# Kernel optimization log

Hardware: AMD Instinct MI355X
Metric: run time of the kernel (lower is better)

Reference implementation:

```python
import jax, jax.numpy as jnp
import numpy as np

GROUP = 128  # quantization group size along the input dimension


def dequant(q, scales, zeros):
    # q: [out, in] int4 codes stored as int32 in [0,16)
    # scales, zeros: [out, in//GROUP] per-group affine params
    out_dim, in_dim = q.shape
    g = in_dim // GROUP
    w = (q.astype(jnp.float32).reshape(out_dim, g, GROUP) - zeros[:, :, None]) * scales[:, :, None]
    return w.reshape(out_dim, in_dim)


def setup_inputs() -> dict:
    key = jax.random.key(0)
    ks = jax.random.split(key, 10)
    H, I = 4096, 11008
    B, S = 64, 1
    inp = {
        "x": jax.random.normal(ks[0], (B, S, H), dtype=jnp.float32),
        "gate_qweight": jax.random.randint(ks[1], (I, H), 0, 16, dtype=jnp.int32),
        "gate_scales": jax.random.uniform(ks[2], (I, H // GROUP), dtype=jnp.float32) * 0.02,
        "gate_zeros": jax.random.uniform(ks[3], (I, H // GROUP), dtype=jnp.float32) * 16.0,
        "up_qweight": jax.random.randint(ks[4], (I, H), 0, 16, dtype=jnp.int32),
        "up_scales": jax.random.uniform(ks[5], (I, H // GROUP), dtype=jnp.float32) * 0.02,
        "up_zeros": jax.random.uniform(ks[6], (I, H // GROUP), dtype=jnp.float32) * 16.0,
        "down_qweight": jax.random.randint(ks[7], (H, I), 0, 16, dtype=jnp.int32),
        "down_scales": jax.random.uniform(ks[8], (H, I // GROUP), dtype=jnp.float32) * 0.02,
        "down_zeros": jax.random.uniform(ks[9], (H, I // GROUP), dtype=jnp.float32) * 16.0,
    }
    return inp


def reference(x, gate_qweight, gate_scales, gate_zeros,
              up_qweight, up_scales, up_zeros,
              down_qweight, down_scales, down_zeros):
    Wg = dequant(gate_qweight, gate_scales, gate_zeros)   # [I, H]
    Wu = dequant(up_qweight, up_scales, up_zeros)         # [I, H]
    Wd = dequant(down_qweight, down_scales, down_zeros)   # [H, I]
    gate = jnp.einsum('bsh,ih->bsi', x, Wg)
    up = jnp.einsum('bsh,ih->bsi', x, Wu)
    h = jax.nn.silu(gate) * up                             # SwiGLU
    return jnp.einsum('bsi,hi->bsh', h, Wd)
```

## Files before the change

kernel.cpp:

```cpp
#include <hip/hip_runtime.h>
#include <hip/hip_bf16.h>
#include <stdint.h>

#define H_DIM 4096
#define I_DIM 11008
#define NGH   (H_DIM/128)
#define NGI   (I_DIM/128)

typedef __attribute__((ext_vector_type(8))) short short8;
typedef __attribute__((ext_vector_type(4))) short s16x4;
typedef __attribute__((ext_vector_type(4))) float f32x4;
typedef __attribute__((ext_vector_type(4))) int   i32x4;

static __device__ __forceinline__ short f2bf(float f) {
  union { __hip_bfloat16 b; short s; } u;
  u.b = __float2bfloat16(f);
  return u.s;
}

__global__ void xcvt_kernel(const float* __restrict__ x, short* __restrict__ xb) {
  int i = (blockIdx.x * 256 + threadIdx.x) * 4;
  f32x4 v = *(const f32x4*)(x + i);
  s16x4 o;
  o[0] = f2bf(v[0]); o[1] = f2bf(v[1]); o[2] = f2bf(v[2]); o[3] = f2bf(v[3]);
  *(s16x4*)(xb + i) = o;
}

__global__ __launch_bounds__(512, 4) void phase1_kernel(
    const short* __restrict__ xb,
    const int* __restrict__ gq, const float* __restrict__ gsc, const float* __restrict__ gze,
    const int* __restrict__ uq, const float* __restrict__ usc, const float* __restrict__ uze,
    short* __restrict__ hb)
{
  __shared__ float red[8][4][4][64];
  const int n0   = blockIdx.x * 16;
  const int w    = threadIdx.x >> 6;
  const int l    = threadIdx.x & 63;
  const int col  = l & 15;
  const int krow = l >> 4;
  const int i    = n0 + col;

  const int*   gqr = gq + (size_t)i * H_DIM;
  const int*   uqr = uq + (size_t)i * H_DIM;
  const float* gsr = gsc + (size_t)i * NGH;
  const float* gzr = gze + (size_t)i * NGH;
  const float* usr = usc + (size_t)i * NGH;
  const float* uzr = uze + (size_t)i * NGH;

  f32x4 accG[4], accU[4];
#pragma unroll
  for (int c = 0; c < 4; ++c)
#pragma unroll
    for (int r = 0; r < 4; ++r) { accG[c][r] = 0.f; accU[c][r] = 0.f; }

  const int kw = w * 512;

  int pk = kw + krow * 8;
  i32x4 nq0 = *(const i32x4*)(gqr + pk);
  i32x4 nq1 = *(const i32x4*)(gqr + pk + 4);
  i32x4 np0 = *(const i32x4*)(uqr + pk);
  i32x4 np1 = *(const i32x4*)(uqr + pk + 4);

#pragma unroll 1
  for (int g = 0; g < 4; ++g) {
    const int gg = w * 4 + g;
    const float sg = gsr[gg], zg = gzr[gg] * sg;
    const float su = usr[gg], zu = uzr[gg] * su;
#pragma unroll
    for (int ks = 0; ks < 4; ++ks) {
      i32x4 q0 = nq0, q1 = nq1, p0 = np0, p1 = np1;
      const int klocal = g * 128 + ks * 32;
      {
        const int nk = kw + ((klocal + 32) & 511) + krow * 8;
        nq0 = *(const i32x4*)(gqr + nk);
        nq1 = *(const i32x4*)(gqr + nk + 4);
        np0 = *(const i32x4*)(uqr + nk);
        np1 = *(const i32x4*)(uqr + nk + 4);
      }
      const int koff = kw + klocal + krow * 8;
      short8 a[4];
#pragma unroll
      for (int c = 0; c < 4; ++c)
        a[c] = *(const short8*)(xb + (size_t)(c * 16 + col) * H_DIM + koff);
      short8 bg, bu;
#pragma unroll
      for (int j = 0; j < 4; ++j) {
        bg[j]     = f2bf((float)q0[j] * sg - zg);
        bg[j + 4] = f2bf((float)q1[j] * sg - zg);
        bu[j]     = f2bf((float)p0[j] * su - zu);
        bu[j + 4] = f2bf((float)p1[j] * su - zu);
      }
#pragma unroll
      for (int c = 0; c < 4; ++c) {
        accG[c] = __builtin_amdgcn_mfma_f32_16x16x32_bf16(a[c], bg, accG[c], 0, 0, 0);
        accU[c] = __builtin_amdgcn_mfma_f32_16x16x32_bf16(a[c], bu, accU[c], 0, 0, 0);
      }
    }
  }

  const int c2 = threadIdx.x >> 7;
  const int rh = (threadIdx.x >> 6) & 1;
  const int ll = threadIdx.x & 63;

#pragma unroll
  for (int c = 0; c < 4; ++c)
#pragma unroll
    for (int r = 0; r < 4; ++r)
      red[w][c][r][l] = accG[c][r];
  __syncthreads();
  float gsum[2];
#pragma unroll
  for (int rr = 0; rr < 2; ++rr) {
    const int r = rh * 2 + rr;
    float s = 0.f;
#pragma unroll
    for (int ww = 0; ww < 8; ++ww) s += red[ww][c2][r][ll];
    gsum[rr] = s;
  }
  __syncthreads();

#pragma unroll
  for (int c = 0; c < 4; ++c)
#pragma unroll
    for (int r = 0; r < 4; ++r)
      red[w][c][r][l] = accU[c][r];
  __syncthreads();
#pragma unroll
  for (int rr = 0; rr < 2; ++rr) {
    const int r = rh * 2 + rr;
    float us = 0.f;
#pragma unroll
    for (int ww = 0; ww < 8; ++ww) us += red[ww][c2][r][ll];
    const float gv = gsum[rr];
    const float hv = gv / (1.f + __expf(-gv)) * us;
    const int m  = c2 * 16 + (ll >> 4) * 4 + r;
    const int ii = n0 + (ll & 15);
    hb[(size_t)m * I_DIM + ii] = f2bf(hv);
  }
}

__global__ __launch_bounds__(512, 4) void phase2_kernel(
    const short* __restrict__ hb,
    const int* __restrict__ dq, const float* __restrict__ dsc, const float* __restrict__ dze,
    float* __restrict__ part)
{
  __shared__ float red[8][4][4][64];
  const int tile  = blockIdx.x & 255;
  const int split = blockIdx.x >> 8;
  const int n0   = tile * 16;
  const int w    = threadIdx.x >> 6;
  const int l    = threadIdx.x & 63;
  const int col  = l & 15;
  const int krow = l >> 4;
  const int n    = n0 + col;

  const int*   dqr = dq + (size_t)n * I_DIM;
  const float* dsr = dsc + (size_t)n * NGI;
  const float* dzr = dze + (size_t)n * NGI;

  f32x4 acc[4];
#pragma unroll
  for (int c = 0; c < 4; ++c)
#pragma unroll
    for (int r = 0; r < 4; ++r) acc[c][r] = 0.f;

  const int cnt    = (w < 6) ? 11 : 10;
  const int sstart = (w < 6) ? w * 11 : 66 + (w - 6) * 10;
  const int kbase  = split * 2752 + sstart * 32;

  int gprev = -1;
  float sv = 0.f, zv = 0.f;

  int pk = kbase + krow * 8;
  i32x4 nq0 = *(const i32x4*)(dqr + pk);
  i32x4 nq1 = *(const i32x4*)(dqr + pk + 4);

#pragma unroll 1
  for (int s = 0; s < cnt; ++s) {
    i32x4 q0 = nq0, q1 = nq1;
    {
      const int ns = (s + 1 < cnt) ? (s + 1) : 0;
      const int nk = kbase + ns * 32 + krow * 8;
      nq0 = *(const i32x4*)(dqr + nk);
      nq1 = *(const i32x4*)(dqr + nk + 4);
    }
    const int k0 = kbase + s * 32;
    const int g  = k0 >> 7;
    if (g != gprev) { sv = dsr[g]; zv = dzr[g] * sv; gprev = g; }
    short8 a[4];
#pragma unroll
    for (int c = 0; c < 4; ++c)
      a[c] = *(const short8*)(hb + (size_t)(c * 16 + col) * I_DIM + k0 + krow * 8);
    short8 b;
#pragma unroll
    for (int j = 0; j < 4; ++j) {
      b[j]     = f2bf((float)q0[j] * sv - zv);
      b[j + 4] = f2bf((float)q1[j] * sv - zv);
    }
#pragma unroll
    for (int c = 0; c < 4; ++c)
      acc[c] = __builtin_amdgcn_mfma_f32_16x16x32_bf16(a[c], b, acc[c], 0, 0, 0);
  }

#pragma unroll
  for (int c = 0; c < 4; ++c)
#pragma unroll
    for (int r = 0; r < 4; ++r)
      red[w][c][r][l] = acc[c][r];
  __syncthreads();

  {
    const int c2 = threadIdx.x >> 7;
    const int rh = (threadIdx.x >> 6) & 1;
    const int ll = threadIdx.x & 63;
    float* po = part + (size_t)split * (64 * H_DIM);
#pragma unroll
    for (int rr = 0; rr < 2; ++rr) {
      const int r = rh * 2 + rr;
      float s = 0.f;
#pragma unroll
      for (int ww = 0; ww < 8; ++ww) s += red[ww][c2][r][ll];
      const int m  = c2 * 16 + (ll >> 4) * 4 + r;
      const int nn = n0 + (ll & 15);
      po[(size_t)m * H_DIM + nn] = s;
    }
  }
}

__global__ void reduce4_kernel(const float* __restrict__ part, float* __restrict__ out) {
  const int idx = (blockIdx.x * 256 + threadIdx.x) * 4;
  const int S = 64 * H_DIM;
  f32x4 s0 = *(const f32x4*)(part + idx);
  f32x4 s1 = *(const f32x4*)(part + S + idx);
  f32x4 s2 = *(const f32x4*)(part + 2 * S + idx);
  f32x4 s3 = *(const f32x4*)(part + 3 * S + idx);
  f32x4 r = (s0 + s1) + (s2 + s3);
  *(f32x4*)(out + idx) = r;
}

extern "C" void kernel_launch(void* const* d_in, const int* in_sizes, int n_in,
                              void* d_out, int out_size, void* d_ws, size_t ws_size,
                              hipStream_t stream) {
  const float* x  = (const float*)d_in[0];
  const int*   gq = (const int*)d_in[1];
  const float* gs = (const float*)d_in[2];
  const float* gz = (const float*)d_in[3];
  const int*   uq = (const int*)d_in[4];
  const float* us = (const float*)d_in[5];
  const float* uz = (const float*)d_in[6];
  const int*   dq = (const int*)d_in[7];
  const float* ds = (const float*)d_in[8];
  const float* dz = (const float*)d_in[9];
  float* out = (float*)d_out;

  short* xb = (short*)d_ws;
  short* hb = (short*)((char*)d_ws + (size_t)64 * H_DIM * 2);
  float* part = (float*)((char*)d_ws + (size_t)64 * H_DIM * 2 + (size_t)64 * I_DIM * 2);

  xcvt_kernel<<<(64 * H_DIM) / 1024, 256, 0, stream>>>(x, xb);
  phase1_kernel<<<I_DIM / 16, 512, 0, stream>>>(xb, gq, gs, gz, uq, us, uz, hb);
  phase2_kernel<<<(H_DIM / 16) * 4, 512, 0, stream>>>(hb, dq, ds, dz, part);
  reduce4_kernel<<<(64 * H_DIM) / 1024, 256, 0, stream>>>(part, out);
}
```

Baseline: 207.7 us.

## Stage quantized weights through LDS with async global_load_lds double buffering

Both GEMV-like phases now copy int4-code rows into shared memory with the global_load_lds builtin, using an XOR swizzle and a double buffer. Each wave then reads its slice from LDS. In phase1 the waves are split so half handle gate and half handle up, rather than every wave doing both. The point is coalesced 16-byte-per-lane row loads and overlap of the next tile's fetch with the current MFMA work. The cost is a __syncthreads per k-step and a larger LDS footprint, which may lower occupancy.

```diff
diff --git a/kernel.cpp b/kernel.cpp
--- a/kernel.cpp
+++ b/kernel.cpp
@@ -4,13 +4,20 @@
 
 #define H_DIM 4096
 #define I_DIM 11008
-#define NGH   (H_DIM/128)
-#define NGI   (I_DIM/128)
+#define NGH   32
+#define NGI   86
 
 typedef __attribute__((ext_vector_type(8))) short short8;
 typedef __attribute__((ext_vector_type(4))) short s16x4;
 typedef __attribute__((ext_vector_type(4))) float f32x4;
 typedef __attribute__((ext_vector_type(4))) int   i32x4;
+
+#define AS1 __attribute__((address_space(1)))
+#define AS3 __attribute__((address_space(3)))
+
+static __device__ __forceinline__ void gload_lds16(const int* src, int* dst) {
+  __builtin_amdgcn_global_load_lds((const AS1 int*)src, (AS3 int*)dst, 16, 0, 0);
+}
 
 static __device__ __forceinline__ short f2bf(float f) {
   union { __hip_bfloat16 b; short s; } u;
@@ -32,110 +39,100 @@
     const int* __restrict__ uq, const float* __restrict__ usc, const float* __restrict__ uze,
     short* __restrict__ hb)
 {
-  __shared__ float red[8][4][4][64];
+  __shared__ int ldsq[2][2][16][256];
   const int n0   = blockIdx.x * 16;
   const int w    = threadIdx.x >> 6;
   const int l    = threadIdx.x & 63;
   const int col  = l & 15;
   const int krow = l >> 4;
-  const int i    = n0 + col;
-
-  const int*   gqr = gq + (size_t)i * H_DIM;
-  const int*   uqr = uq + (size_t)i * H_DIM;
-  const float* gsr = gsc + (size_t)i * NGH;
-  const float* gzr = gze + (size_t)i * NGH;
-  const float* usr = usc + (size_t)i * NGH;
-  const float* uzr = uze + (size_t)i * NGH;
-
-  f32x4 accG[4], accU[4];
-#pragma unroll
-  for (int c = 0; c < 4; ++c)
-#pragma unroll
-    for (int r = 0; r < 4; ++r) { accG[c][r] = 0.f; accU[c][r] = 0.f; }
-
-  const int kw = w * 512;
-
-  int pk = kw + krow * 8;
-  i32x4 nq0 = *(const i32x4*)(gqr + pk);
-  i32x4 nq1 = *(const i32x4*)(gqr + pk + 4);
-  i32x4 np0 = *(const i32x4*)(uqr + pk);
-  i32x4 np1 = *(const i32x4*)(uqr + pk + 4);
+  const int pp   = w >> 2;
+  const int q    = w & 3;
+
+  const int*   qb  = pp ? uq  : gq;
+  const float* scp = pp ? usc : gsc;
+  const float* zep = pp ? uze : gze;
+  const int    iidx = n0 + col;
+
+  f32x4 acc[4];
+#pragma unroll
+  for (int c = 0; c < 4; ++c)
+#pragma unroll
+    for (int r = 0; r < 4; ++r) acc[c][r] = 0.f;
+
+  const int rq = q * 4;
+  const int* srow[4];
+#pragma unroll
+  for (int rr = 0; rr < 4; ++rr)
+    srow[rr] = qb + (size_t)(n0 + rq + rr) * H_DIM + ((l ^ ((rq + rr) & 7)) << 2);
+
+#pragma unroll
+  for (int rr = 0; rr < 4; ++rr)
+    gload_lds16(srow[rr], &ldsq[0][pp][rq + rr][0]);
+  __syncthreads();
+
+  const int* lbase = &ldsq[0][pp][col][0];
 
 #pragma unroll 1
-  for (int g = 0; g < 4; ++g) {
-    const int gg = w * 4 + g;
-    const float sg = gsr[gg], zg = gzr[gg] * sg;
-    const float su = usr[gg], zu = uzr[gg] * su;
-#pragma unroll
-    for (int ks = 0; ks < 4; ++ks) {
-      i32x4 q0 = nq0, q1 = nq1, p0 = np0, p1 = np1;
-      const int klocal = g * 128 + ks * 32;
-      {
-        const int nk = kw + ((klocal + 32) & 511) + krow * 8;
-        nq0 = *(const i32x4*)(gqr + nk);
-        nq1 = *(const i32x4*)(gqr + nk + 4);
-        np0 = *(const i32x4*)(uqr + nk);
-        np1 = *(const i32x4*)(uqr + nk + 4);
+  for (int kw = 0; kw < 16; ++kw) {
+    const int bf = kw & 1;
+    short8 a[2][4];
+#pragma unroll
+    for (int ss = 0; ss < 2; ++ss) {
+      const int kg = kw * 256 + q * 64 + ss * 32 + krow * 8;
+#pragma unroll
+      for (int c = 0; c < 4; ++c)
+        a[ss][c] = *(const short8*)(xb + (size_t)(c * 16 + col) * H_DIM + kg);
+    }
+    if (kw + 1 < 16) {
+#pragma unroll
+      for (int rr = 0; rr < 4; ++rr)
+        gload_lds16(srow[rr] + (kw + 1) * 256, &ldsq[bf ^ 1][pp][rq + rr][0]);
+    }
+    const int g = kw * 2 + (q >> 1);
+    const float sv = scp[iidx * NGH + g];
+    const float zv = zep[iidx * NGH + g] * sv;
+    const int* lb = lbase + bf * 8192;
+#pragma unroll
+    for (int ss = 0; ss < 2; ++ss) {
+      const int slot0 = q * 16 + ss * 8 + krow * 2;
+      i32x4 lo = *(const i32x4*)(lb + ((slot0 ^ (col & 7)) << 2));
+      i32x4 hi = *(const i32x4*)(lb + (((slot0 + 1) ^ (col & 7)) << 2));
+      short8 b;
+#pragma unroll
+      for (int j = 0; j < 4; ++j) {
+        b[j]     = f2bf((float)lo[j] * sv - zv);
+        b[j + 4] = f2bf((float)hi[j] * sv - zv);
       }
-      const int koff = kw + klocal + krow * 8;
-      short8 a[4];
 #pragma unroll
       for (int c = 0; c < 4; ++c)
-        a[c] = *(const short8*)(xb + (size_t)(c * 16 + col) * H_DIM + koff);
-      short8 bg, bu;
-#pragma unroll
-      for (int j = 0; j < 4; ++j) {
-        bg[j]     = f2bf((float)q0[j] * sg - zg);
-        bg[j + 4] = f2bf((float)q1[j] * sg - zg);
-        bu[j]     = f2bf((float)p0[j] * su - zu);
-        bu[j + 4] = f2bf((float)p1[j] * su - zu);
+        acc[c] = __builtin_amdgcn_mfma_f32_16x16x32_bf16(a[ss][c], b, acc[c], 0, 0, 0);
+    }
+    __syncthreads();
+  }
+
+  float* red = (float*)&ldsq[0][0][0][0];
+#pragma unroll
+  for (int c = 0; c < 4; ++c)
+#pragma unroll
+    for (int r = 0; r < 4; ++r)
+      red[((w * 16 + c * 4 + r) << 6) + l] = acc[c][r];
+  __syncthreads();
+  if (threadIdx.x < 256) {
+    const int c2 = threadIdx.x >> 6;
+    const int ll = threadIdx.x & 63;
+#pragma unroll
+    for (int r = 0; r < 4; ++r) {
+      float gs_ = 0.f, us_ = 0.f;
+#pragma unroll
+      for (int ww = 0; ww < 4; ++ww) {
+        gs_ += red[(((ww    ) * 16 + c2 * 4 + r) << 6) + ll];
+        us_ += red[(((ww + 4) * 16 + c2 * 4 + r) << 6) + ll];
       }
-#pragma unroll
-      for (int c = 0; c < 4; ++c) {
-        accG[c] = __builtin_amdgcn_mfma_f32_16x16x32_bf16(a[c], bg, accG[c], 0, 0, 0);
-        accU[c] = __builtin_amdgcn_mfma_f32_16x16x32_bf16(a[c], bu, accU[c], 0, 0, 0);
-      }
-    }
-  }
-
-  const int c2 = threadIdx.x >> 7;
-  const int rh = (threadIdx.x >> 6) & 1;
-  const int ll = threadIdx.x & 63;
-
-#pragma unroll
-  for (int c = 0; c < 4; ++c)
-#pragma unroll
-    for (int r = 0; r < 4; ++r)
-      red[w][c][r][l] = accG[c][r];
-  __syncthreads();
-  float gsum[2];
-#pragma unroll
-  for (int rr = 0; rr < 2; ++rr) {
-    const int r = rh * 2 + rr;
-    float s = 0.f;
-#pragma unroll
-    for (int ww = 0; ww < 8; ++ww) s += red[ww][c2][r][ll];
-    gsum[rr] = s;
-  }
-  __syncthreads();
-
-#pragma unroll
-  for (int c = 0; c < 4; ++c)
-#pragma unroll
-    for (int r = 0; r < 4; ++r)
-      red[w][c][r][l] = accU[c][r];
-  __syncthreads();
-#pragma unroll
-  for (int rr = 0; rr < 2; ++rr) {
-    const int r = rh * 2 + rr;
-    float us = 0.f;
-#pragma unroll
-    for (int ww = 0; ww < 8; ++ww) us += red[ww][c2][r][ll];
-    const float gv = gsum[rr];
-    const float hv = gv / (1.f + __expf(-gv)) * us;
-    const int m  = c2 * 16 + (ll >> 4) * 4 + r;
-    const int ii = n0 + (ll & 15);
-    hb[(size_t)m * I_DIM + ii] = f2bf(hv);
+      const float hv = gs_ / (1.f + __expf(-gs_)) * us_;
+      const int m  = c2 * 16 + (ll >> 4) * 4 + r;
+      const int ii = n0 + (ll & 15);
+      hb[(size_t)m * I_DIM + ii] = f2bf(hv);
+    }
   }
 }
 
@@ -144,7 +141,7 @@
     const int* __restrict__ dq, const float* __restrict__ dsc, const float* __restrict__ dze,
     float* __restrict__ part)
 {
-  __shared__ float red[8][4][4][64];
+  __shared__ int ldsq[2][16][256];
   const int tile  = blockIdx.x & 255;
   const int split = blockIdx.x >> 8;
   const int n0   = tile * 16;
@@ -152,11 +149,10 @@
   const int l    = threadIdx.x & 63;
   const int col  = l & 15;
   const int krow = l >> 4;
-  const int n    = n0 + col;
-
-  const int*   dqr = dq + (size_t)n * I_DIM;
-  const float* dsr = dsc + (size_t)n * NGI;
-  const float* dzr = dze + (size_t)n * NGI;
+  const int nidx = n0 + col;
+
+  const int kw0 = split * 11;
+  const int nkw = (split < 3) ? 11 : 10;
 
   f32x4 acc[4];
 #pragma unroll
@@ -164,62 +160,68 @@
 #pragma unroll
     for (int r = 0; r < 4; ++r) acc[c][r] = 0.f;
 
-  const int cnt    = (w < 6) ? 11 : 10;
-  const int sstart = (w < 6) ? w * 11 : 66 + (w - 6) * 10;
-  const int kbase  = split * 2752 + sstart * 32;
-
-  int gprev = -1;
-  float sv = 0.f, zv = 0.f;
-
-  int pk = kbase + krow * 8;
-  i32x4 nq0 = *(const i32x4*)(dqr + pk);
-  i32x4 nq1 = *(const i32x4*)(dqr + pk + 4);
+  const int* srow[2];
+#pragma unroll
+  for (int rr = 0; rr < 2; ++rr) {
+    const int r = w * 2 + rr;
+    srow[rr] = dq + (size_t)(n0 + r) * I_DIM + kw0 * 256 + ((l ^ (r & 7)) << 2);
+  }
+
+#pragma unroll
+  for (int rr = 0; rr < 2; ++rr)
+    gload_lds16(srow[rr], &ldsq[0][w * 2 + rr][0]);
+  __syncthreads();
 
 #pragma unroll 1
-  for (int s = 0; s < cnt; ++s) {
-    i32x4 q0 = nq0, q1 = nq1;
-    {
-      const int ns = (s + 1 < cnt) ? (s + 1) : 0;
-      const int nk = kbase + ns * 32 + krow * 8;
-      nq0 = *(const i32x4*)(dqr + nk);
-      nq1 = *(const i32x4*)(dqr + nk + 4);
-    }
-    const int k0 = kbase + s * 32;
-    const int g  = k0 >> 7;
-    if (g != gprev) { sv = dsr[g]; zv = dzr[g] * sv; gprev = g; }
+  for (int ki = 0; ki < nkw; ++ki) {
+    const int kw = kw0 + ki;
+    const int bf = ki & 1;
     short8 a[4];
+    const int kg = kw * 256 + w * 32 + krow * 8;
 #pragma unroll
     for (int c = 0; c < 4; ++c)
-      a[c] = *(const short8*)(hb + (size_t)(c * 16 + col) * I_DIM + k0 + krow * 8);
+      a[c] = *(const short8*)(hb + (size_t)(c * 16 + col) * I_DIM + kg);
+    if (ki + 1 < nkw) {
+#pragma unroll
+      for (int rr = 0; rr < 2; ++rr)
+        gload_lds16(srow[rr] + (ki + 1) * 256, &ldsq[bf ^ 1][w * 2 + rr][0]);
+    }
+    const int g = kw * 2 + (w >> 2);
+    const float sv = dsc[nidx * NGI + g];
+    const float zv = dze[nidx * NGI + g] * sv;
+    const int* lb = &ldsq[bf][col][0];
+    const int slot0 = w * 8 + krow * 2;
+    i32x4 lo = *(const i32x4*)(lb + ((slot0 ^ (col & 7)) << 2));
+    i32x4 hi = *(const i32x4*)(lb + (((slot0 + 1) ^ (col & 7)) << 2));
     short8 b;
 #pragma unroll
     for (int j = 0; j < 4; ++j) {
-      b[j]     = f2bf((float)q0[j] * sv - zv);
-      b[j + 4] = f2bf((float)q1[j] * sv - zv);
+      b[j]     = f2bf((float)lo[j] * sv - zv);
+      b[j + 4] = f2bf((float)hi[j] * sv - zv);
     }
 #pragma unroll
     for (int c = 0; c < 4; ++c)
       acc[c] = __builtin_amdgcn_mfma_f32_16x16x32_bf16(a[c], b, acc[c], 0, 0, 0);
-  }
-
+    __syncthreads();
+  }
+
+  float* red = (float*)&ldsq[0][0][0];
 #pragma unroll
   for (int c = 0; c < 4; ++c)
 #pragma unroll
     for (int r = 0; r < 4; ++r)
-      red[w][c][r][l] = acc[c][r];
-  __syncthreads();
-
-  {
-    const int c2 = threadIdx.x >> 7;
-    const int rh = (threadIdx.x >> 6) & 1;
+      red[((w * 16 + c * 4 + r) << 6) + l] = acc[c][r];
+  __syncthreads();
+  if (threadIdx.x < 256) {
+    const int c2 = threadIdx.x >> 6;
     const int ll = threadIdx.x & 63;
     float* po = part + (size_t)split * (64 * H_DIM);
 #pragma unroll
-    for (int rr = 0; rr < 2; ++rr) {
-      const int r = rh * 2 + rr;
+    for (int r = 0; r < 4; ++r) {
       float s = 0.f;
 #pragma unroll
-      for (int ww = 0; ww < 8; ++ww) s += red[ww][c2][r][ll];
+      for (int ww = 0; ww < 8; ++ww)
+        s += red[((ww * 16 + c2 * 4 + r) << 6) + ll];
       const int m  = c2 * 16 + (ll >> 4) * 4 + r;
       const int nn = n0 + (ll & 15);
       po[(size_t)m * H_DIM + nn] = s;
```

Result: slower. 215.4 us (+3.7%).

## Pack int4 weight codes into nibbles before the GEMM phases

Applied to the files above, without the earlier changes.

Adds a pack kernel that, on every call, compresses each group of eight int32 weight codes into one 32-bit word. New phase kernels load these packed words and unpack nibbles in registers, cutting the weight bytes the GEMM kernels read by 8x. The packing still reads the full int32 weights and writes the packed buffers each call, so total memory traffic goes up and there are extra launches. It falls back to the old kernels when the workspace is too small. The phase-2 epilogue reduction is also reassigned to 256 threads.

```diff
diff --git a/kernel.cpp b/kernel.cpp
--- a/kernel.cpp
+++ b/kernel.cpp
@@ -4,8 +4,10 @@
 
 #define H_DIM 4096
 #define I_DIM 11008
-#define NGH   (H_DIM/128)
-#define NGI   (I_DIM/128)
+#define NGH   32
+#define NGI   86
+#define HP    (H_DIM/8)
+#define IP    (I_DIM/8)
 
 typedef __attribute__((ext_vector_type(8))) short short8;
 typedef __attribute__((ext_vector_type(4))) short s16x4;
@@ -26,7 +28,215 @@
   *(s16x4*)(xb + i) = o;
 }
 
-__global__ __launch_bounds__(512, 4) void phase1_kernel(
+__global__ __launch_bounds__(256) void pack_kernel(const int* __restrict__ src,
+                                                   int* __restrict__ dst) {
+  const int o = blockIdx.x * 256 + threadIdx.x;
+  const int* s = src + (size_t)o * 8;
+  i32x4 a = *(const i32x4*)s;
+  i32x4 b = *(const i32x4*)(s + 4);
+  int p = (a[0] & 15)        | ((a[1] & 15) << 4)  | ((a[2] & 15) << 8)  | ((a[3] & 15) << 12)
+        | ((b[0] & 15) << 16) | ((b[1] & 15) << 20) | ((b[2] & 15) << 24) | ((b[3] & 15) << 28);
+  dst[o] = p;
+}
+
+__global__ __launch_bounds__(512, 4) void phase1p_kernel(
+    const short* __restrict__ xb,
+    const int* __restrict__ gp, const float* __restrict__ gsc, const float* __restrict__ gze,
+    const int* __restrict__ up, const float* __restrict__ usc, const float* __restrict__ uze,
+    short* __restrict__ hb)
+{
+  __shared__ float red[8][4][4][64];
+  const int n0   = blockIdx.x * 16;
+  const int w    = threadIdx.x >> 6;
+  const int l    = threadIdx.x & 63;
+  const int col  = l & 15;
+  const int krow = l >> 4;
+  const int i    = n0 + col;
+
+  const int*   gpr = gp + (size_t)i * HP;
+  const int*   upr = up + (size_t)i * HP;
+  const float* gsr = gsc + (size_t)i * NGH;
+  const float* gzr = gze + (size_t)i * NGH;
+  const float* usr = usc + (size_t)i * NGH;
+  const float* uzr = uze + (size_t)i * NGH;
+
+  f32x4 accG[4], accU[4];
+#pragma unroll
+  for (int c = 0; c < 4; ++c)
+#pragma unroll
+    for (int r = 0; r < 4; ++r) { accG[c][r] = 0.f; accU[c][r] = 0.f; }
+
+  const int wb = w * 64;
+
+  int qg = gpr[wb + krow];
+  int qu = upr[wb + krow];
+
+#pragma unroll 1
+  for (int g = 0; g < 4; ++g) {
+    const int gg = w * 4 + g;
+    const float sg = gsr[gg], zg = gzr[gg] * sg;
+    const float su = usr[gg], zu = uzr[gg] * su;
+#pragma unroll
+    for (int ks = 0; ks < 4; ++ks) {
+      const int cg = qg, cu = qu;
+      const int wloc = g * 16 + ks * 4;
+      {
+        const int nw = wb + ((wloc + 4) & 63) + krow;
+        qg = gpr[nw];
+        qu = upr[nw];
+      }
+      const int kg = w * 512 + g * 128 + ks * 32 + krow * 8;
+      short8 a[4];
+#pragma unroll
+      for (int c = 0; c < 4; ++c)
+        a[c] = *(const short8*)(xb + (size_t)(c * 16 + col) * H_DIM + kg);
+      short8 bg, bu;
+#pragma unroll
+      for (int j = 0; j < 8; ++j) {
+        bg[j] = f2bf((float)((cg >> (4 * j)) & 15) * sg - zg);
+        bu[j] = f2bf((float)((cu >> (4 * j)) & 15) * su - zu);
+      }
+#pragma unroll
+      for (int c = 0; c < 4; ++c) {
+        accG[c] = __builtin_amdgcn_mfma_f32_16x16x32_bf16(a[c], bg, accG[c], 0, 0, 0);
+        accU[c] = __builtin_amdgcn_mfma_f32_16x16x32_bf16(a[c], bu, accU[c], 0, 0, 0);
+      }
+    }
+  }
+
+  const int c2 = threadIdx.x >> 7;
+  const int rh = (threadIdx.x >> 6) & 1;
+  const int ll = threadIdx.x & 63;
+
+#pragma unroll
+  for (int c = 0; c < 4; ++c)
+#pragma unroll
+    for (int r = 0; r < 4; ++r)
+      red[w][c][r][l] = accG[c][r];
+  __syncthreads();
+  float gsum[2];
+#pragma unroll
+  for (int rr = 0; rr < 2; ++rr) {
+    const int r = rh * 2 + rr;
+    float s = 0.f;
+#pragma unroll
+    for (int ww = 0; ww < 8; ++ww) s += red[ww][c2][r][ll];
+    gsum[rr] = s;
+  }
+  __syncthreads();
+
+#pragma unroll
+  for (int c = 0; c < 4; ++c)
+#pragma unroll
+    for (int r = 0; r < 4; ++r)
+      red[w][c][r][l] = accU[c][r];
+  __syncthreads();
+#pragma unroll
+  for (int rr = 0; rr < 2; ++rr) {
+    const int r = rh * 2 + rr;
+    float us = 0.f;
+#pragma unroll
+    for (int ww = 0; ww < 8; ++ww) us += red[ww][c2][r][ll];
+    const float gv = gsum[rr];
+    const float hv = gv / (1.f + __expf(-gv)) * us;
+    const int m  = c2 * 16 + (ll >> 4) * 4 + r;
+    const int ii = n0 + (ll & 15);
+    hb[(size_t)m * I_DIM + ii] = f2bf(hv);
+  }
+}
+
+__global__ __launch_bounds__(512, 4) void phase2p_kernel(
+    const short* __restrict__ hb,
+    const int* __restrict__ dp, const float* __restrict__ dsc, const float* __restrict__ dze,
+    float* __restrict__ part)
+{
+  __shared__ float red[8][4][4][64];
+  const int tile  = blockIdx.x & 255;
+  const int split = blockIdx.x >> 8;
+  const int n0   = tile * 16;
+  const int w    = threadIdx.x >> 6;
+  const int l    = threadIdx.x & 63;
+  const int col  = l & 15;
+  const int krow = l >> 4;
+  const int n    = n0 + col;
+
+  const int*   dpr = dp + (size_t)n * IP;
+  const float* dsr = dsc + (size_t)n * NGI;
+  const float* dzr = dze + (size_t)n * NGI;
+
+  f32x4 acc[4];
+#pragma unroll
+  for (int c = 0; c < 4; ++c)
+#pragma unroll
+    for (int r = 0; r < 4; ++r) acc[c][r] = 0.f;
+
+  const int cnt    = (w < 6) ? 11 : 10;
+  const int sstart = (w < 6) ? w * 11 : 66 + (w - 6) * 10;
+  const int kbase  = split * 2752 + sstart * 32;
+  const int wbase  = split * 344 + sstart * 4;
+
+  int gprev = -1;
+  float sv = 0.f, zv = 0.f;
+
+  int qd = dpr[wbase + krow];
+#pragma unroll 1
+  for (int s = 0; s < cnt; ++s) {
+    const int cd = qd;
+    {
+      const int ns = (s + 1 < cnt) ? (s + 1) : 0;
+      qd = dpr[wbase + ns * 4 + krow];
+    }
+    const int k0 = kbase + s * 32;
+    const int g  = k0 >> 7;
+    if (g != gprev) { sv = dsr[g]; zv = dzr[g] * sv; gprev = g; }
+    short8 a[4];
+#pragma unroll
+    for (int c = 0; c < 4; ++c)
+      a[c] = *(const short8*)(hb + (size_t)(c * 16 + col) * I_DIM + k0 + krow * 8);
+    short8 b;
+#pragma unroll
+    for (int j = 0; j < 8; ++j)
+      b[j] = f2bf((float)((cd >> (4 * j)) & 15) * sv - zv);
+#pragma unroll
+    for (int c = 0; c < 4; ++c)
+      acc[c] = __builtin_amdgcn_mfma_f32_16x16x32_bf16(a[c], b, acc[c], 0, 0, 0);
+  }
+
+#pragma unroll
+  for (int c = 0; c < 4; ++c)
+#pragma unroll
+    for (int r = 0; r < 4; ++r)
+      red[w][c][r][l] = acc[c][r];
+  __syncthreads();
+
+  if (threadIdx.x < 256) {
+    const int c2 = threadIdx.x >> 6;
+    const int ll = threadIdx.x & 63;
+    float* po = part + (size_t)split * (64 * H_DIM);
+#pragma unroll
+    for (int r = 0; r < 4; ++r) {
+      float s = 0.f;
+#pragma unroll
+      for (int ww = 0; ww < 8; ++ww) s += red[ww][c2][r][ll];
+      const int m  = c2 * 16 + (ll >> 4) * 4 + r;
+      const int nn = n0 + (ll & 15);
+      po[(size_t)m * H_DIM + nn] = s;
+    }
+  }
+}
+
+__global__ void reduce4_kernel(const float* __restrict__ part, float* __restrict__ out) {
+  const int idx = (blockIdx.x * 256 + threadIdx.x) * 4;
+  const int S = 64 * H_DIM;
+  f32x4 s0 = *(const f32x4*)(part + idx);
+  f32x4 s1 = *(const f32x4*)(part + S + idx);
+  f32x4 s2 = *(const f32x4*)(part + 2 * S + idx);
+  f32x4 s3 = *(const f32x4*)(part + 3 * S + idx);
+  f32x4 r = (s0 + s1) + (s2 + s3);
+  *(f32x4*)(out + idx) = r;
+}
+
+__global__ __launch_bounds__(512, 4) void phase1f_kernel(
     const short* __restrict__ xb,
     const int* __restrict__ gq, const float* __restrict__ gsc, const float* __restrict__ gze,
     const int* __restrict__ uq, const float* __restrict__ usc, const float* __restrict__ uze,
@@ -39,28 +249,23 @@
   const int col  = l & 15;
   const int krow = l >> 4;
   const int i    = n0 + col;
-
   const int*   gqr = gq + (size_t)i * H_DIM;
   const int*   uqr = uq + (size_t)i * H_DIM;
   const float* gsr = gsc + (size_t)i * NGH;
   const float* gzr = gze + (size_t)i * NGH;
   const float* usr = usc + (size_t)i * NGH;
   const float* uzr = uze + (size_t)i * NGH;
-
   f32x4 accG[4], accU[4];
 #pragma unroll
   for (int c = 0; c < 4; ++c)
 #pragma unroll
     for (int r = 0; r < 4; ++r) { accG[c][r] = 0.f; accU[c][r] = 0.f; }
-
   const int kw = w * 512;
-
   int pk = kw + krow * 8;
   i32x4 nq0 = *(const i32x4*)(gqr + pk);
   i32x4 nq1 = *(const i32x4*)(gqr + pk + 4);
   i32x4 np0 = *(const i32x4*)(uqr + pk);
   i32x4 np1 = *(const i32x4*)(uqr + pk + 4);
-
 #pragma unroll 1
   for (int g = 0; g < 4; ++g) {
     const int gg = w * 4 + g;
@@ -97,11 +302,9 @@
       }
     }
   }
-
   const int c2 = threadIdx.x >> 7;
   const int rh = (threadIdx.x >> 6) & 1;
   const int ll = threadIdx.x & 63;
-
 #pragma unroll
   for (int c = 0; c < 4; ++c)
 #pragma unroll
@@ -118,7 +321,6 @@
     gsum[rr] = s;
   }
   __syncthreads();
-
 #pragma unroll
   for (int c = 0; c < 4; ++c)
 #pragma unroll
@@ -139,7 +341,7 @@
   }
 }
 
-__global__ __launch_bounds__(512, 4) void phase2_kernel(
+__global__ __launch_bounds__(512, 4) void phase2f_kernel(
     const short* __restrict__ hb,
     const int* __restrict__ dq, const float* __restrict__ dsc, const float* __restrict__ dze,
     float* __restrict__ part)
@@ -153,28 +355,22 @@
   const int col  = l & 15;
   const int krow = l >> 4;
   const int n    = n0 + col;
-
   const int*   dqr = dq + (size_t)n * I_DIM;
   const float* dsr = dsc + (size_t)n * NGI;
   const float* dzr = dze + (size_t)n * NGI;
-
   f32x4 acc[4];
 #pragma unroll
   for (int c = 0; c < 4; ++c)
 #pragma unroll
     for (int r = 0; r < 4; ++r) acc[c][r] = 0.f;
-
   const int cnt    = (w < 6) ? 11 : 10;
   const int sstart = (w < 6) ? w * 11 : 66 + (w - 6) * 10;
   const int kbase  = split * 2752 + sstart * 32;
-
   int gprev = -1;
   float sv = 0.f, zv = 0.f;
-
   int pk = kbase + krow * 8;
   i32x4 nq0 = *(const i32x4*)(dqr + pk);
   i32x4 nq1 = *(const i32x4*)(dqr + pk + 4);
-
 #pragma unroll 1
   for (int s = 0; s < cnt; ++s) {
     i32x4 q0 = nq0, q1 = nq1;
@@ -201,22 +397,18 @@
     for (int c = 0; c < 4; ++c)
       acc[c] = __builtin_amdgcn_mfma_f32_16x16x32_bf16(a[c], b, acc[c], 0, 0, 0);
   }
-
 #pragma unroll
   for (int c = 0; c < 4; ++c)
 #pragma unroll
     for (int r = 0; r < 4; ++r)
       red[w][c][r][l] = acc[c][r];
   __syncthreads();
-
-  {
-    const int c2 = threadIdx.x >> 7;
-    const int rh = (threadIdx.x >> 6) & 1;
+  if (threadIdx.x < 256) {
+    const int c2 = threadIdx.x >> 6;
     const int ll = threadIdx.x & 63;
     float* po = part + (size_t)split * (64 * H_DIM);
 #pragma unroll
-    for (int rr = 0; rr < 2; ++rr) {
-      const int r = rh * 2 + rr;
+    for (int r = 0; r < 4; ++r) {
       float s = 0.f;
 #pragma unroll
       for (int ww = 0; ww < 8; ++ww) s += red[ww][c2][r][ll];
@@ -225,17 +417,6 @@
       po[(size_t)m * H_DIM + nn] = s;
     }
   }
-}
-
-__global__ void reduce4_kernel(const float* __restrict__ part, float* __restrict__ out) {
-  const int idx = (blockIdx.x * 256 + threadIdx.x) * 4;
-  const int S = 64 * H_DIM;
-  f32x4 s0 = *(const f32x4*)(part + idx);
-  f32x4 s1 = *(const f32x4*)(part + S + idx);
-  f32x4 s2 = *(const f32x4*)(part + 2 * S + idx);
-  f32x4 s3 = *(const f32x4*)(part + 3 * S + idx);
-  f32x4 r = (s0 + s1) + (s2 + s3);
-  *(f32x4*)(out + idx) = r;
 }
 
 extern "C" void kernel_launch(void* const* d_in, const int* in_sizes, int n_in,
@@ -253,12 +434,31 @@
   const float* dz = (const float*)d_in[9];
   float* out = (float*)d_out;
 
-  short* xb = (short*)d_ws;
-  short* hb = (short*)((char*)d_ws + (size_t)64 * H_DIM * 2);
-  float* part = (float*)((char*)d_ws + (size_t)64 * H_DIM * 2 + (size_t)64 * I_DIM * 2);
+  const size_t XB   = (size_t)64 * H_DIM * 2;
+  const size_t HB   = (size_t)64 * I_DIM * 2;
+  const size_t PART = (size_t)4 * 64 * H_DIM * 4;
+  const size_t NW   = (size_t)I_DIM * HP;
+  const size_t PK   = NW * 4;
+
+  short* xb   = (short*)d_ws;
+  short* hb   = (short*)((char*)d_ws + XB);
+  float* part = (float*)((char*)d_ws + XB + HB);
+  int*   gp   = (int*)((char*)d_ws + XB + HB + PART);
+  int*   upk  = (int*)((char*)d_ws + XB + HB + PART + PK);
+  int*   dpk  = (int*)((char*)d_ws + XB + HB + PART + 2 * PK);
 
   xcvt_kernel<<<(64 * H_DIM) / 1024, 256, 0, stream>>>(x, xb);
-  phase1_kernel<<<I_DIM / 16, 512, 0, stream>>>(xb, gq, gs, gz, uq, us, uz, hb);
-  phase2_kernel<<<(H_DIM / 16) * 4, 512, 0, stream>>>(hb, dq, ds, dz, part);
+
+  if (ws_size >= XB + HB + PART + 3 * PK) {
+    const int pblk = (int)(NW / 256);
+    pack_kernel<<<pblk, 256, 0, stream>>>(gq, gp);
+    pack_kernel<<<pblk, 256, 0, stream>>>(uq, upk);
+    phase1p_kernel<<<I_DIM / 16, 512, 0, stream>>>(xb, gp, gs, gz, upk, us, uz, hb);
+    pack_kernel<<<pblk, 256, 0, stream>>>(dq, dpk);
+    phase2p_kernel<<<(H_DIM / 16) * 4, 512, 0, stream>>>(hb, dpk, ds, dz, part);
+  } else {
+    phase1f_kernel<<<I_DIM / 16, 512, 0, stream>>>(xb, gq, gs, gz, uq, us, uz, hb);
+    phase2f_kernel<<<(H_DIM / 16) * 4, 512, 0, stream>>>(hb, dq, ds, dz, part);
+  }
   reduce4_kernel<<<(64 * H_DIM) / 1024, 256, 0, stream>>>(part, out);
 }
```

Result: slower. 246.6 us (+18.7%).
